# Performance work log

Hardware: AMD Instinct MI355X
Metric: run time of the kernel (lower is better)

## Reference

```python
import jax, jax.numpy as jnp
import numpy as np

B, I, O, ORDER = 16384, 256, 256, 8
LO, HI = -1.0, 1.0


def setup_inputs() -> dict:
    key = jax.random.key(0)
    k1, k2, k3 = jax.random.split(key, 3)
    x = jax.random.normal(k1, (B, I), dtype=jnp.float32)
    weights = jax.random.normal(k2, (O, I), dtype=jnp.float32)
    # BernsteinBasisFunction init: randn(order+1) * 0.1, one per (o, i) pair
    coeffs = jax.random.normal(k3, (O, I, ORDER + 1), dtype=jnp.float32) * 0.1
    return {"x": x, "weights": weights, "coeffs": coeffs}


def reference(x, weights, coeffs):
    # x: [B, I]; weights: [O, I]; coeffs: [O, I, K+1]
    K = coeffs.shape[-1] - 1
    zoom = (HI - LO) / 2.0
    pan = (HI + LO) / 2.0
    xt = jnp.tanh(x) * zoom + pan          # squash into [LO, HI]
    x_a = xt - LO                          # [B, I]
    x_b = HI - xt                          # [B, I]
    e = jnp.arange(K + 1)
    # ber[b, i, k] = x_a^k * x_b^(K-k)  (unnormalized Bernstein basis)
    ber = (x_a[..., None] ** e) * (x_b[..., None] ** (K - e))  # [B, I, K+1]
    # transformed[b, o, i] = sum_k coeffs[o,i,k] * ber[b,i,k]; out = einsum('boi,oi->bo')
    # Fused: fold weights into coeffs to avoid the [B, O, I] intermediate.
    wc = coeffs * weights[..., None]       # [O, I, K+1]
    return jnp.einsum('bik,oik->bo', ber, wc)
```

## Files before the change

kernel.cpp:

```cpp
#include <hip/hip_runtime.h>
#include <hip/hip_bf16.h>


#define BDIM 16384
#define IDIM 256
#define ODIM 256
#define NK 9
#define NCHUNK 4
#define NSTEP 36
#define STEP_ELEMS (ODIM * 64)

typedef short short8 __attribute__((ext_vector_type(8)));
typedef float floatx4 __attribute__((ext_vector_type(4)));

__global__ __launch_bounds__(256) void prep_wc2(const float* __restrict__ weights,
                                                const float* __restrict__ coeffs,
                                                ushort* __restrict__ wc) {
    int idx  = blockIdx.x * 256 + threadIdx.x;
    int step = idx >> 11;
    int c    = idx & 2047;
    int big    = c >> 6;
    int lane_w = c & 63;
    int o    = (big >> 1) * 16 + (lane_w & 15);
    int s    = big & 1;
    int quad = lane_w >> 4;
    int ic = step / 9;
    int k  = step - ic * 9;
    int i0 = ic * 64 + s * 32 + quad * 8;

    const float* cp = coeffs + (size_t)(o * IDIM + i0) * NK + k;
    float4 w0 = *(const float4*)(weights + o * IDIM + i0);
    float4 w1 = *(const float4*)(weights + o * IDIM + i0 + 4);
    float wv[8] = {w0.x, w0.y, w0.z, w0.w, w1.x, w1.y, w1.z, w1.w};

    union { ushort us[8]; int4 v; __hip_bfloat162 h2[4]; } pk;
#pragma unroll
    for (int j = 0; j < 8; j += 2) {
        float a = cp[(size_t)j * NK] * wv[j];
        float b = cp[(size_t)(j + 1) * NK] * wv[j + 1];
        pk.h2[j >> 1] = __float22bfloat162_rn(make_float2(a, b));
    }
    *(int4*)(wc + (size_t)step * STEP_ELEMS + (size_t)c * 8) = pk.v;
}

__global__ __launch_bounds__(256, 2) void bern_gemm(const float* __restrict__ x,
                                                    const ushort* __restrict__ wc,
                                                    float* __restrict__ out) {
    const int tid  = threadIdx.x;
    const int wave = tid >> 6;
    const int lane = tid & 63;
    const int row0 = blockIdx.x * 32;
    const int lrow = lane & 15;
    const int jseg = (lane >> 4) * 8;

    float p[2][2][8];
    float r[2][2][8];
    float xc[2][2][8];
    floatx4 acc[2][4];
    floatx4 zero = {0.0f, 0.0f, 0.0f, 0.0f};
#pragma unroll
    for (int m = 0; m < 2; ++m)
#pragma unroll
        for (int n = 0; n < 4; ++n)
            acc[m][n] = zero;

#define LOAD_XCHUNK(ic_)                                                        \
    {                                                                           \
        _Pragma("unroll") for (int m = 0; m < 2; ++m)                           \
        _Pragma("unroll") for (int s = 0; s < 2; ++s) {                         \
            const float* xp = x + (size_t)(row0 + m * 16 + lrow) * IDIM         \
                              + (ic_) * 64 + s * 32 + jseg;                     \
            float4 v0 = *(const float4*)(xp);                                   \
            float4 v1 = *(const float4*)(xp + 4);                               \
            xc[m][s][0] = v0.x; xc[m][s][1] = v0.y;                             \
            xc[m][s][2] = v0.z; xc[m][s][3] = v0.w;                             \
            xc[m][s][4] = v1.x; xc[m][s][5] = v1.y;                             \
            xc[m][s][6] = v1.z; xc[m][s][7] = v1.w;                             \
        }                                                                       \
    }

#define SETUP_BASIS()                                                           \
    {                                                                           \
        _Pragma("unroll") for (int m = 0; m < 2; ++m)                           \
        _Pragma("unroll") for (int s = 0; s < 2; ++s)                           \
        _Pragma("unroll") for (int e = 0; e < 8; ++e) {                         \
            float t  = __builtin_amdgcn_exp2f(xc[m][s][e] * 2.8853900817779268f);\
            float q  = 2.0f * __builtin_amdgcn_rcpf(t + 1.0f);                  \
            float q2 = q * q;                                                   \
            float q4 = q2 * q2;                                                 \
            p[m][s][e] = q4 * q4;                                               \
            r[m][s][e] = t;                                                     \
        }                                                                       \
    }

    LOAD_XCHUNK(0);
    SETUP_BASIS();
    LOAD_XCHUNK(1);

    short8 bfr[2][2][4];
    {
        const ushort* w0p = wc;
#pragma unroll
        for (int s = 0; s < 2; ++s)
#pragma unroll
            for (int n = 0; n < 4; ++n)
                bfr[0][s][n] = *(const short8*)(w0p + (((wave * 4 + n) * 2 + s) * 64 + lane) * 8);
    }

#pragma unroll
    for (int ic = 0; ic < NCHUNK; ++ic) {
#pragma unroll
        for (int k = 0; k < NK; ++k) {
            const int step = ic * NK + k;
            const int cur  = step & 1;
            const int nxt  = cur ^ 1;

            if (step + 1 < NSTEP) {
                const ushort* wnp = wc + (size_t)(step + 1) * STEP_ELEMS;
#pragma unroll
                for (int s = 0; s < 2; ++s)
#pragma unroll
                    for (int n = 0; n < 4; ++n)
                        bfr[nxt][s][n] = *(const short8*)(wnp + (((wave * 4 + n) * 2 + s) * 64 + lane) * 8);
            }

            short8 af[2][2];
#pragma unroll
            for (int m = 0; m < 2; ++m)
#pragma unroll
                for (int s = 0; s < 2; ++s) {
                    union { ushort us[8]; short8 v; __hip_bfloat162 h2[4]; } pk;
#pragma unroll
                    for (int e = 0; e < 8; e += 2) {
                        pk.h2[e >> 1] = __float22bfloat162_rn(
                            make_float2(p[m][s][e], p[m][s][e + 1]));
                        p[m][s][e]     *= r[m][s][e];
                        p[m][s][e + 1] *= r[m][s][e + 1];
                    }
                    af[m][s] = pk.v;
                }

#pragma unroll
            for (int s = 0; s < 2; ++s)
#pragma unroll
                for (int m = 0; m < 2; ++m)
#pragma unroll
                    for (int n = 0; n < 4; ++n)
                        acc[m][n] = __builtin_amdgcn_mfma_f32_16x16x32_bf16(
                            af[m][s], bfr[cur][s][n], acc[m][n], 0, 0, 0);
        }

        if (ic < NCHUNK - 1) {
            SETUP_BASIS();
            if (ic < NCHUNK - 2) LOAD_XCHUNK(ic + 2);
        }
    }

#pragma unroll
    for (int m = 0; m < 2; ++m) {
#pragma unroll
        for (int n = 0; n < 4; ++n) {
            int col   = wave * 64 + n * 16 + (lane & 15);
            int rbase = row0 + m * 16 + (lane >> 4) * 4;
#pragma unroll
            for (int reg = 0; reg < 4; ++reg) {
                out[(size_t)(rbase + reg) * ODIM + col] = acc[m][n][reg];
            }
        }
    }
#undef LOAD_XCHUNK
#undef SETUP_BASIS
}

extern "C" void kernel_launch(void* const* d_in, const int* in_sizes, int n_in,
                              void* d_out, int out_size, void* d_ws, size_t ws_size,
                              hipStream_t stream) {
    const float* x       = (const float*)d_in[0];
    const float* weights = (const float*)d_in[1];
    const float* coeffs  = (const float*)d_in[2];
    float* out = (float*)d_out;
    ushort* wc = (ushort*)d_ws;

    prep_wc2<<<288, 256, 0, stream>>>(weights, coeffs, wc);
    bern_gemm<<<BDIM / 32, 256, 0, stream>>>(x, wc, out);
}
```

Before: 106.1 us.

## Use 512-thread blocks with two row halves and drop x-chunk prefetch registers

Doubles the block to 512 threads, so two groups of four waves each cover 32 rows and share the same weight fragments through cache. The separate x prefetch buffer is removed: x is loaded straight into the p registers just before the basis setup, and the A fragments are packed inside the MFMA loop instead of being staged in an af array. The aim is lower register pressure so more waves can be resident, and fewer wc fetches per row. The cost is that the x load is no longer hidden behind compute, which may expose global load latency at every chunk boundary.

```diff
diff --git a/kernel.cpp b/kernel.cpp
--- a/kernel.cpp
+++ b/kernel.cpp
@@ -43,19 +43,20 @@
     *(int4*)(wc + (size_t)step * STEP_ELEMS + (size_t)c * 8) = pk.v;
 }
 
-__global__ __launch_bounds__(256, 2) void bern_gemm(const float* __restrict__ x,
+__global__ __launch_bounds__(512, 2) void bern_gemm(const float* __restrict__ x,
                                                     const ushort* __restrict__ wc,
                                                     float* __restrict__ out) {
     const int tid  = threadIdx.x;
     const int wave = tid >> 6;
     const int lane = tid & 63;
-    const int row0 = blockIdx.x * 32;
+    const int half = wave >> 2;
+    const int wv4  = wave & 3;
+    const int rb   = blockIdx.x * 64 + half * 32;
     const int lrow = lane & 15;
     const int jseg = (lane >> 4) * 8;
 
     float p[2][2][8];
     float r[2][2][8];
-    float xc[2][2][8];
     floatx4 acc[2][4];
     floatx4 zero = {0.0f, 0.0f, 0.0f, 0.0f};
 #pragma unroll
@@ -64,18 +65,18 @@
         for (int n = 0; n < 4; ++n)
             acc[m][n] = zero;
 
-#define LOAD_XCHUNK(ic_)                                                        \
+#define LOAD_X(ic_)                                                             \
     {                                                                           \
         _Pragma("unroll") for (int m = 0; m < 2; ++m)                           \
         _Pragma("unroll") for (int s = 0; s < 2; ++s) {                         \
-            const float* xp = x + (size_t)(row0 + m * 16 + lrow) * IDIM         \
+            const float* xp = x + (size_t)(rb + m * 16 + lrow) * IDIM           \
                               + (ic_) * 64 + s * 32 + jseg;                     \
             float4 v0 = *(const float4*)(xp);                                   \
             float4 v1 = *(const float4*)(xp + 4);                               \
-            xc[m][s][0] = v0.x; xc[m][s][1] = v0.y;                             \
-            xc[m][s][2] = v0.z; xc[m][s][3] = v0.w;                             \
-            xc[m][s][4] = v1.x; xc[m][s][5] = v1.y;                             \
-            xc[m][s][6] = v1.z; xc[m][s][7] = v1.w;                             \
+            p[m][s][0] = v0.x; p[m][s][1] = v0.y;                               \
+            p[m][s][2] = v0.z; p[m][s][3] = v0.w;                               \
+            p[m][s][4] = v1.x; p[m][s][5] = v1.y;                               \
+            p[m][s][6] = v1.z; p[m][s][7] = v1.w;                               \
         }                                                                       \
     }
 
@@ -84,7 +85,7 @@
         _Pragma("unroll") for (int m = 0; m < 2; ++m)                           \
         _Pragma("unroll") for (int s = 0; s < 2; ++s)                           \
         _Pragma("unroll") for (int e = 0; e < 8; ++e) {                         \
-            float t  = __builtin_amdgcn_exp2f(xc[m][s][e] * 2.8853900817779268f);\
+            float t  = __builtin_amdgcn_exp2f(p[m][s][e] * 2.8853900817779268f);\
             float q  = 2.0f * __builtin_amdgcn_rcpf(t + 1.0f);                  \
             float q2 = q * q;                                                   \
             float q4 = q2 * q2;                                                 \
@@ -93,19 +94,15 @@
         }                                                                       \
     }
 
-    LOAD_XCHUNK(0);
+    LOAD_X(0);
     SETUP_BASIS();
-    LOAD_XCHUNK(1);
 
     short8 bfr[2][2][4];
-    {
-        const ushort* w0p = wc;
 #pragma unroll
-        for (int s = 0; s < 2; ++s)
+    for (int s = 0; s < 2; ++s)
 #pragma unroll
-            for (int n = 0; n < 4; ++n)
-                bfr[0][s][n] = *(const short8*)(w0p + (((wave * 4 + n) * 2 + s) * 64 + lane) * 8);
-    }
+        for (int n = 0; n < 4; ++n)
+            bfr[0][s][n] = *(const short8*)(wc + (((wv4 * 4 + n) * 2 + s) * 64 + lane) * 8);
 
 #pragma unroll
     for (int ic = 0; ic < NCHUNK; ++ic) {
@@ -121,38 +118,32 @@
                 for (int s = 0; s < 2; ++s)
 #pragma unroll
                     for (int n = 0; n < 4; ++n)
-                        bfr[nxt][s][n] = *(const short8*)(wnp + (((wave * 4 + n) * 2 + s) * 64 + lane) * 8);
+                        bfr[nxt][s][n] = *(const short8*)(wnp + (((wv4 * 4 + n) * 2 + s) * 64 + lane) * 8);
             }
 
-            short8 af[2][2];
 #pragma unroll
-            for (int m = 0; m < 2; ++m)
+            for (int s = 0; s < 2; ++s)
 #pragma unroll
-                for (int s = 0; s < 2; ++s) {
+                for (int m = 0; m < 2; ++m) {
                     union { ushort us[8]; short8 v; __hip_bfloat162 h2[4]; } pk;
 #pragma unroll
                     for (int e = 0; e < 8; e += 2) {
                         pk.h2[e >> 1] = __float22bfloat162_rn(
                             make_float2(p[m][s][e], p[m][s][e + 1]));
-                        p[m][s][e]     *= r[m][s][e];
-                        p[m][s][e + 1] *= r[m][s][e + 1];
                     }
-                    af[m][s] = pk.v;
-                }
-
-#pragma unroll
-            for (int s = 0; s < 2; ++s)
-#pragma unroll
-                for (int m = 0; m < 2; ++m)
 #pragma unroll
                     for (int n = 0; n < 4; ++n)
                         acc[m][n] = __builtin_amdgcn_mfma_f32_16x16x32_bf16(
-                            af[m][s], bfr[cur][s][n], acc[m][n], 0, 0, 0);
+                            pk.v, bfr[cur][s][n], acc[m][n], 0, 0, 0);
+                    if (k < NK - 1)
+#pragma unroll
+                        for (int e = 0; e < 8; ++e) p[m][s][e] *= r[m][s][e];
+                }
         }
 
         if (ic < NCHUNK - 1) {
+            LOAD_X(ic + 1);
             SETUP_BASIS();
-            if (ic < NCHUNK - 2) LOAD_XCHUNK(ic + 2);
         }
     }
 
@@ -160,15 +151,15 @@
     for (int m = 0; m < 2; ++m) {
 #pragma unroll
         for (int n = 0; n < 4; ++n) {
-            int col   = wave * 64 + n * 16 + (lane & 15);
-            int rbase = row0 + m * 16 + (lane >> 4) * 4;
+            int col   = wv4 * 64 + n * 16 + (lane & 15);
+            int rbase = rb + m * 16 + (lane >> 4) * 4;
 #pragma unroll
             for (int reg = 0; reg < 4; ++reg) {
                 out[(size_t)(rbase + reg) * ODIM + col] = acc[m][n][reg];
             }
         }
     }
-#undef LOAD_XCHUNK
+#undef LOAD_X
 #undef SETUP_BASIS
 }
 
@@ -182,5 +173,5 @@
     ushort* wc = (ushort*)d_ws;
 
     prep_wc2<<<288, 256, 0, stream>>>(weights, coeffs, wc);
-    bern_gemm<<<BDIM / 32, 256, 0, stream>>>(x, wc, out);
+    bern_gemm<<<BDIM / 64, 512, 0, stream>>>(x, wc, out);
 }
```

Result: no change. 107.6 us (+1.4%).
